# Optimization experiments

Hardware: AMD Instinct MI355X
Metric: run time of the kernel (lower is better)

## Reference

```python
import jax, jax.numpy as jnp
import numpy as np

F = 16        # num_frames
K = 8         # num_tokens (top-k)
SIZE = 64     # basis size
PD = 256      # prompt_dim
ED = 768      # embed_dim
EPS = 1e-12

def _l2norm(v, axis=-1):
    n = jnp.sqrt(jnp.sum(v * v, axis=axis, keepdims=True))
    return v / jnp.maximum(n, EPS)

def setup_inputs() -> dict:
    key = jax.random.key(0)
    k1, k2, k3, k4 = jax.random.split(key, 4)
    B, N = 32, 197
    x = jax.random.normal(k1, (B, F * N, ED), dtype=jnp.float32)
    # prompt_values ~ U(-1, 1), shape [size, 1, prompt_dim]
    prompt_values = jax.random.uniform(k2, (SIZE, 1, PD), dtype=jnp.float32, minval=-1.0, maxval=1.0)
    # prompt_inproj: Linear(embed_dim, prompt_dim, bias=False)
    W_in = jax.random.normal(k3, (PD, ED), dtype=jnp.float32) * (1.0 / np.sqrt(ED))
    # prompt_outproj: Linear(prompt_dim, embed_dim, bias=False), kaiming fan_out
    W_out = jax.random.normal(k4, (ED, PD), dtype=jnp.float32) * np.sqrt(2.0 / ED)
    return {"x": x, "W_in": W_in, "W_out": W_out, "prompt_values": prompt_values}

def reference(x, W_in, W_out, prompt_values):
    B = x.shape[0]
    x = jax.lax.stop_gradient(x)                       # x.detach()
    xf = x.reshape(B, F, -1, ED).mean(axis=2)          # [B, F, ED]
    query = jnp.einsum('bfe,pe->bfp', xf, W_in)        # prompt_inproj
    BZ = B * F
    q = _l2norm(query.reshape(BZ, PD), axis=1)         # [BZ, PD]
    keys = _l2norm(prompt_values.mean(axis=1), axis=1) # [SIZE, PD]
    sim = q @ keys.T                                   # [BZ, SIZE]
    # eval routing: top-k by similarity (argsort descending [:, :k])
    _, idx = jax.lax.top_k(sim, K)                     # [BZ, K] int32
    prompts = prompt_values[idx.reshape(-1)].reshape(BZ, K, PD)
    prompts = _l2norm(prompts, axis=-1)
    sel_sim = jnp.take_along_axis(sim, idx, axis=1)    # [BZ, K]
    sel_key = keys[idx]                                # [BZ, K, PD]
    recon = jnp.einsum('bk,bkd->bd', sel_sim, sel_key) # [BZ, PD]
    diff = jnp.sum((recon - jax.lax.stop_gradient(q)) ** 2) / BZ
    ksim = jnp.sum(jnp.abs(keys @ keys.T - jnp.eye(SIZE, dtype=keys.dtype))) / BZ
    ps = diff + ksim
    # rearrange '(b f) p d -> b (f p) d' then outproj
    out_prompts = prompts.reshape(B, F * K, PD)
    out_prompts = jnp.einsum('bnd,ed->bne', out_prompts, W_out)  # [B, F*K, ED]
    ps_loss = jnp.zeros((1,), dtype=x.dtype) + ps * F
    return out_prompts, ps_loss
```

## Files before the change

### kernel.cpp

```cpp
#include <hip/hip_runtime.h>

#define Ff 16
#define Kk 8
#define SIZEk 64
#define PDd 256
#define EDd 768
#define Nn 197
#define BZz 512
#define NPROD 64
#define RB  256
#define ED4 192
#define PD4 64
#define OUT_LOSS ((size_t)32 * 128 * EDd)
#define LOSS_SCALE (1.0f / 32.0f)
#define MAGIC 0x5A17EC0Du

__device__ __forceinline__ void acc4(float4& s, float4 a) {
    s.x += a.x; s.y += a.y; s.z += a.z; s.w += a.w;
}

__global__ __launch_bounds__(256, 2) void k_all(const float4* __restrict__ x,
                                                const float* __restrict__ Win,
                                                const float* __restrict__ Wout,
                                                const float* __restrict__ pv,
                                                float* __restrict__ keys,
                                                float* __restrict__ KW,
                                                unsigned* __restrict__ slots,
                                                float* __restrict__ out) {
    int blk = blockIdx.x, t = threadIdx.x;

    if (blk < NPROD) {
        __shared__ float ks[PDd];
        __shared__ float redp[4];
        __shared__ float s_norm;
        int s = blk;
        float v  = pv[(size_t)s * PDd + t];
        float sq = v * v;
        for (int o = 32; o > 0; o >>= 1) sq += __shfl_down(sq, o);
        if ((t & 63) == 0) redp[t >> 6] = sq;
        __syncthreads();
        if (t == 0) s_norm = fmaxf(sqrtf(redp[0] + redp[1] + redp[2] + redp[3]), 1e-12f);
        __syncthreads();
        float kv = v / s_norm;
        ks[t] = kv;
        keys[(size_t)s * PDd + t] = kv;
        __syncthreads();

        for (int r = 0; r < 3; r++) {
            int e = t + 256 * r;
            const float4* w  = (const float4*)(Wout + (size_t)e * PDd);
            const float4* k4 = (const float4*)ks;
            float d = 0.f;
            for (int i = 0; i < PD4; i++) {
                float4 wv = w[i]; float4 kvv = k4[i];
                d += wv.x * kvv.x + wv.y * kvv.y + wv.z * kvv.z + wv.w * kvv.w;
            }
            KW[(size_t)s * EDd + e] = d;
        }
        if (s == 0 && t == 0) out[OUT_LOSS] = 0.0f;
        __syncthreads();
        if (t == 0)
            __hip_atomic_store(&slots[s], MAGIC, __ATOMIC_RELEASE, __HIP_MEMORY_SCOPE_AGENT);

        if (t < SIZEk) {
            while (__hip_atomic_load(&slots[t], __ATOMIC_ACQUIRE, __HIP_MEMORY_SCOPE_AGENT)
                   != MAGIC)
                __builtin_amdgcn_s_sleep(8);
        }
        __syncthreads();
        if (t < SIZEk) {
            const float4* a = (const float4*)(keys + (size_t)s * PDd);
            const float4* b = (const float4*)(keys + (size_t)t * PDd);
            float d = 0.f;
            for (int c = 0; c < PD4; c++) {
                float4 av = a[c], bv = b[c];
                d += av.x * bv.x + av.y * bv.y + av.z * bv.z + av.w * bv.w;
            }
            float vv = fabsf(d - (s == t ? 1.0f : 0.0f));
            for (int o = 32; o > 0; o >>= 1) vv += __shfl_down(vv, o);
            if (t == 0) atomicAdd(out + OUT_LOSS, vv * LOSS_SCALE);
        }
        return;
    }

    __shared__ float xs[2][EDd];
    __shared__ float qs[2][PDd];
    __shared__ int   s_idx[2][Kk];
    __shared__ float s_sim[2][Kk];
    __shared__ float red[2][4];
    int bz0 = (blk - NPROD) * 2;

    {
        const float4* b0 = x + (size_t)bz0 * Nn * ED4;
        const float4* b1 = b0 + (size_t)Nn * ED4;
        const int  rA = (t < ED4) ? 0 : 1;
        const int  cA = (t < ED4) ? t : (t - ED4);
        const float4* pA = (rA ? b1 : b0) + cA;
        const bool hasB = (t < 128);
        const int  cB   = 64 + (t & 127);
        const float4* pB = b1 + cB;
        float4 sA = make_float4(0.f, 0.f, 0.f, 0.f);
        float4 sB = make_float4(0.f, 0.f, 0.f, 0.f);
        int n = 0;
        if (hasB) {
            for (; n + 8 <= Nn; n += 8) {
                float4 a0 = pA[(n + 0) * ED4], a1 = pA[(n + 1) * ED4];
                float4 a2 = pA[(n + 2) * ED4], a3 = pA[(n + 3) * ED4];
                float4 a4 = pA[(n + 4) * ED4], a5 = pA[(n + 5) * ED4];
                float4 a6 = pA[(n + 6) * ED4], a7 = pA[(n + 7) * ED4];
                float4 q0 = pB[(n + 0) * ED4], q1 = pB[(n + 1) * ED4];
                float4 q2 = pB[(n + 2) * ED4], q3 = pB[(n + 3) * ED4];
                float4 q4 = pB[(n + 4) * ED4], q5 = pB[(n + 5) * ED4];
                float4 q6 = pB[(n + 6) * ED4], q7 = pB[(n + 7) * ED4];
                acc4(sA, a0); acc4(sA, a1); acc4(sA, a2); acc4(sA, a3);
                acc4(sA, a4); acc4(sA, a5); acc4(sA, a6); acc4(sA, a7);
                acc4(sB, q0); acc4(sB, q1); acc4(sB, q2); acc4(sB, q3);
                acc4(sB, q4); acc4(sB, q5); acc4(sB, q6); acc4(sB, q7);
            }
            for (; n < Nn; n++) { acc4(sA, pA[n * ED4]); acc4(sB, pB[n * ED4]); }
        } else {
            for (; n + 8 <= Nn; n += 8) {
                float4 a0 = pA[(n + 0) * ED4], a1 = pA[(n + 1) * ED4];
                float4 a2 = pA[(n + 2) * ED4], a3 = pA[(n + 3) * ED4];
                float4 a4 = pA[(n + 4) * ED4], a5 = pA[(n + 5) * ED4];
                float4 a6 = pA[(n + 6) * ED4], a7 = pA[(n + 7) * ED4];
                acc4(sA, a0); acc4(sA, a1); acc4(sA, a2); acc4(sA, a3);
                acc4(sA, a4); acc4(sA, a5); acc4(sA, a6); acc4(sA, a7);
            }
            for (; n < Nn; n++) acc4(sA, pA[n * ED4]);
        }
        const float inv = 1.0f / (float)Nn;
        ((float4*)xs[rA])[cA] = make_float4(sA.x * inv, sA.y * inv, sA.z * inv, sA.w * inv);
        if (hasB)
            ((float4*)xs[1])[cB] = make_float4(sB.x * inv, sB.y * inv, sB.z * inv, sB.w * inv);
    }
    __syncthreads();

    {
        const float4* w  = (const float4*)Win + (size_t)t * ED4;
        const float4* x0 = (const float4*)xs[0];
        const float4* x1 = (const float4*)xs[1];
        float d0a = 0.f, d0b = 0.f, d1a = 0.f, d1b = 0.f;
        for (int i = 0; i < ED4; i += 2) {
            float4 w0 = w[i],     w1 = w[i + 1];
            float4 u0 = x0[i],    u1 = x1[i];
            float4 u2 = x0[i + 1], u3 = x1[i + 1];
            d0a += w0.x * u0.x + w0.y * u0.y + w0.z * u0.z + w0.w * u0.w;
            d1a += w0.x * u1.x + w0.y * u1.y + w0.z * u1.z + w0.w * u1.w;
            d0b += w1.x * u2.x + w1.y * u2.y + w1.z * u2.z + w1.w * u2.w;
            d1b += w1.x * u3.x + w1.y * u3.y + w1.z * u3.z + w1.w * u3.w;
        }
        float d0 = d0a + d0b, d1 = d1a + d1b;
        float sq0 = d0 * d0, sq1 = d1 * d1;
        for (int o = 32; o > 0; o >>= 1) {
            sq0 += __shfl_down(sq0, o);
            sq1 += __shfl_down(sq1, o);
        }
        if ((t & 63) == 0) { red[0][t >> 6] = sq0; red[1][t >> 6] = sq1; }
        __syncthreads();
        float n0 = fmaxf(sqrtf(red[0][0] + red[0][1] + red[0][2] + red[0][3]), 1e-12f);
        float n1 = fmaxf(sqrtf(red[1][0] + red[1][1] + red[1][2] + red[1][3]), 1e-12f);
        qs[0][t] = d0 / n0;
        qs[1][t] = d1 / n1;
    }

    if (t < SIZEk) {
        while (__hip_atomic_load(&slots[t], __ATOMIC_ACQUIRE, __HIP_MEMORY_SCOPE_AGENT)
               != MAGIC)
            __builtin_amdgcn_s_sleep(8);
    }
    __syncthreads();

    if (t < 2 * SIZEk) {
        int row  = t >> 6;
        int lane = t & 63;
        const float4* kr = (const float4*)(keys + (size_t)lane * PDd);
        const float4* qr = (const float4*)qs[row];
        float d = 0.f;
        for (int c = 0; c < PD4; c++) {
            float4 a = kr[c], b = qr[c];
            d += a.x * b.x + a.y * b.y + a.z * b.z + a.w * b.w;
        }
        float v = d;
        for (int k = 0; k < Kk; k++) {
            float mv = v; int mi = lane;
            for (int o = 32; o > 0; o >>= 1) {
                float ov = __shfl_xor(mv, o);
                int   oi = __shfl_xor(mi, o);
                if (ov > mv || (ov == mv && oi < mi)) { mv = ov; mi = oi; }
            }
            if (lane == 0) { s_idx[row][k] = mi; s_sim[row][k] = mv; }
            if (lane == mi) v = -3e38f;
        }
    }
    __syncthreads();

    {
        float r0 = 0.f, r1 = 0.f;
        for (int k = 0; k < Kk; k++) {
            r0 += s_sim[0][k] * keys[(size_t)s_idx[0][k] * PDd + t];
            r1 += s_sim[1][k] * keys[(size_t)s_idx[1][k] * PDd + t];
        }
        float e0 = r0 - qs[0][t];
        float e1 = r1 - qs[1][t];
        float sq = e0 * e0 + e1 * e1;
        for (int o = 32; o > 0; o >>= 1) sq += __shfl_down(sq, o);
        if ((t & 63) == 0) red[0][t >> 6] = sq;
        __syncthreads();
        if (t == 0) atomicAdd(out + OUT_LOSS,
                              (red[0][0] + red[0][1] + red[0][2] + red[0][3]) * LOSS_SCALE);
    }

    float4* orow = (float4*)out + (size_t)bz0 * Kk * ED4;
    for (int i = t; i < 2 * Kk * ED4; i += 256) {
        int which = i / ED4;
        int e4    = i - which * ED4;
        int idx   = s_idx[which >> 3][which & 7];
        orow[i] = ((const float4*)(KW + (size_t)idx * EDd))[e4];
    }
}

extern "C" void kernel_launch(void* const* d_in, const int* in_sizes, int n_in,
                              void* d_out, int out_size, void* d_ws, size_t ws_size,
                              hipStream_t stream) {
    const float* x    = (const float*)d_in[0];
    const float* Win  = (const float*)d_in[1];
    const float* Wout = (const float*)d_in[2];
    const float* pv   = (const float*)d_in[3];
    float* out = (float*)d_out;
    float* ws  = (float*)d_ws;

    float*    keys  = ws;
    float*    KW    = ws + 16384;
    unsigned* slots = (unsigned*)(ws + 65536);

    k_all<<<NPROD + RB, 256, 0, stream>>>((const float4*)x, Win, Wout, pv,
                                          keys, KW, slots, out);
}
```

Measured before the change: 502.9 us.

## Split frame-mean into a separate high-parallelism kernel before routing kernel

The single fused kernel is split into two launches. The first computes key normalisation plus the per-frame token mean, using 1536 blocks (three column chunks per frame, four row-groups per block). The second does the projection, top-k routing and output gather from the stored means. This spreads the ~194MB streaming read of x across many more blocks than the previous 256 to raise memory-level parallelism. It also removes the in-kernel spin-wait on key slots, at the cost of an extra launch and a small workspace round trip.

```diff
diff --git a/kernel.cpp b/kernel.cpp
--- a/kernel.cpp
+++ b/kernel.cpp
@@ -8,6 +8,7 @@
 #define Nn 197
 #define BZz 512
 #define NPROD 64
+#define NMEAN 1536
 #define RB  256
 #define ED4 192
 #define PD4 64
@@ -19,14 +20,14 @@
     s.x += a.x; s.y += a.y; s.z += a.z; s.w += a.w;
 }
 
-__global__ __launch_bounds__(256, 2) void k_all(const float4* __restrict__ x,
-                                                const float* __restrict__ Win,
-                                                const float* __restrict__ Wout,
-                                                const float* __restrict__ pv,
-                                                float* __restrict__ keys,
-                                                float* __restrict__ KW,
-                                                unsigned* __restrict__ slots,
-                                                float* __restrict__ out) {
+__global__ __launch_bounds__(256, 4) void k_mean(const float4* __restrict__ x,
+                                                 const float* __restrict__ Wout,
+                                                 const float* __restrict__ pv,
+                                                 float* __restrict__ keys,
+                                                 float* __restrict__ KW,
+                                                 unsigned* __restrict__ slots,
+                                                 float4* __restrict__ xf,
+                                                 float* __restrict__ out) {
     int blk = blockIdx.x, t = threadIdx.x;
 
     if (blk < NPROD) {
@@ -83,56 +84,57 @@
         return;
     }
 
+    int m  = blk - NPROD;
+    int bz = m / 3;
+    int c3 = m - bz * 3;
+    int c = t & 63, g = t >> 6;
+    const int STR = 4 * ED4;
+    const float4* p = x + ((size_t)bz * Nn + g) * ED4 + c3 * 64 + c;
+    float4 s = make_float4(0.f, 0.f, 0.f, 0.f);
+    int cnt = (Nn - g + 3) >> 2;
+    int j = 0;
+    for (; j + 8 <= cnt; j += 8) {
+        float4 a0 = p[(size_t)(j + 0) * STR], a1 = p[(size_t)(j + 1) * STR];
+        float4 a2 = p[(size_t)(j + 2) * STR], a3 = p[(size_t)(j + 3) * STR];
+        float4 a4 = p[(size_t)(j + 4) * STR], a5 = p[(size_t)(j + 5) * STR];
+        float4 a6 = p[(size_t)(j + 6) * STR], a7 = p[(size_t)(j + 7) * STR];
+        acc4(s, a0); acc4(s, a1); acc4(s, a2); acc4(s, a3);
+        acc4(s, a4); acc4(s, a5); acc4(s, a6); acc4(s, a7);
+    }
+    for (; j < cnt; j++) acc4(s, p[(size_t)j * STR]);
+
+    __shared__ float4 part[4][64];
+    part[g][c] = s;
+    __syncthreads();
+    if (t < 64) {
+        float4 a = part[0][t], b = part[1][t], d2 = part[2][t], e = part[3][t];
+        const float inv = 1.0f / (float)Nn;
+        float4 r;
+        r.x = (a.x + b.x + d2.x + e.x) * inv;
+        r.y = (a.y + b.y + d2.y + e.y) * inv;
+        r.z = (a.z + b.z + d2.z + e.z) * inv;
+        r.w = (a.w + b.w + d2.w + e.w) * inv;
+        xf[(size_t)bz * ED4 + c3 * 64 + t] = r;
+    }
+}
+
+__global__ __launch_bounds__(256, 2) void k_route(const float* __restrict__ Win,
+                                                  const float* __restrict__ keys,
+                                                  const float* __restrict__ KW,
+                                                  const float4* __restrict__ xf,
+                                                  float* __restrict__ out) {
+    int blk = blockIdx.x, t = threadIdx.x;
     __shared__ float xs[2][EDd];
     __shared__ float qs[2][PDd];
     __shared__ int   s_idx[2][Kk];
     __shared__ float s_sim[2][Kk];
     __shared__ float red[2][4];
-    int bz0 = (blk - NPROD) * 2;
+    int bz0 = blk * 2;
 
     {
-        const float4* b0 = x + (size_t)bz0 * Nn * ED4;
-        const float4* b1 = b0 + (size_t)Nn * ED4;
-        const int  rA = (t < ED4) ? 0 : 1;
-        const int  cA = (t < ED4) ? t : (t - ED4);
-        const float4* pA = (rA ? b1 : b0) + cA;
-        const bool hasB = (t < 128);
-        const int  cB   = 64 + (t & 127);
-        const float4* pB = b1 + cB;
-        float4 sA = make_float4(0.f, 0.f, 0.f, 0.f);
-        float4 sB = make_float4(0.f, 0.f, 0.f, 0.f);
-        int n = 0;
-        if (hasB) {
-            for (; n + 8 <= Nn; n += 8) {
-                float4 a0 = pA[(n + 0) * ED4], a1 = pA[(n + 1) * ED4];
-                float4 a2 = pA[(n + 2) * ED4], a3 = pA[(n + 3) * ED4];
-                float4 a4 = pA[(n + 4) * ED4], a5 = pA[(n + 5) * ED4];
-                float4 a6 = pA[(n + 6) * ED4], a7 = pA[(n + 7) * ED4];
-                float4 q0 = pB[(n + 0) * ED4], q1 = pB[(n + 1) * ED4];
-                float4 q2 = pB[(n + 2) * ED4], q3 = pB[(n + 3) * ED4];
-                float4 q4 = pB[(n + 4) * ED4], q5 = pB[(n + 5) * ED4];
-                float4 q6 = pB[(n + 6) * ED4], q7 = pB[(n + 7) * ED4];
-                acc4(sA, a0); acc4(sA, a1); acc4(sA, a2); acc4(sA, a3);
-                acc4(sA, a4); acc4(sA, a5); acc4(sA, a6); acc4(sA, a7);
-                acc4(sB, q0); acc4(sB, q1); acc4(sB, q2); acc4(sB, q3);
-                acc4(sB, q4); acc4(sB, q5); acc4(sB, q6); acc4(sB, q7);
-            }
-            for (; n < Nn; n++) { acc4(sA, pA[n * ED4]); acc4(sB, pB[n * ED4]); }
-        } else {
-            for (; n + 8 <= Nn; n += 8) {
-                float4 a0 = pA[(n + 0) * ED4], a1 = pA[(n + 1) * ED4];
-                float4 a2 = pA[(n + 2) * ED4], a3 = pA[(n + 3) * ED4];
-                float4 a4 = pA[(n + 4) * ED4], a5 = pA[(n + 5) * ED4];
-                float4 a6 = pA[(n + 6) * ED4], a7 = pA[(n + 7) * ED4];
-                acc4(sA, a0); acc4(sA, a1); acc4(sA, a2); acc4(sA, a3);
-                acc4(sA, a4); acc4(sA, a5); acc4(sA, a6); acc4(sA, a7);
-            }
-            for (; n < Nn; n++) acc4(sA, pA[n * ED4]);
-        }
-        const float inv = 1.0f / (float)Nn;
-        ((float4*)xs[rA])[cA] = make_float4(sA.x * inv, sA.y * inv, sA.z * inv, sA.w * inv);
-        if (hasB)
-            ((float4*)xs[1])[cB] = make_float4(sB.x * inv, sB.y * inv, sB.z * inv, sB.w * inv);
+        const float4* src = xf + (size_t)bz0 * ED4;
+        for (int i = t; i < 2 * ED4; i += 256)
+            ((float4*)xs)[i] = src[i];
     }
     __syncthreads();
 
@@ -142,8 +144,8 @@
         const float4* x1 = (const float4*)xs[1];
         float d0a = 0.f, d0b = 0.f, d1a = 0.f, d1b = 0.f;
         for (int i = 0; i < ED4; i += 2) {
-            float4 w0 = w[i],     w1 = w[i + 1];
-            float4 u0 = x0[i],    u1 = x1[i];
+            float4 w0 = w[i],      w1 = w[i + 1];
+            float4 u0 = x0[i],     u1 = x1[i];
             float4 u2 = x0[i + 1], u3 = x1[i + 1];
             d0a += w0.x * u0.x + w0.y * u0.y + w0.z * u0.z + w0.w * u0.w;
             d1a += w0.x * u1.x + w0.y * u1.y + w0.z * u1.z + w0.w * u1.w;
@@ -162,12 +164,6 @@
         float n1 = fmaxf(sqrtf(red[1][0] + red[1][1] + red[1][2] + red[1][3]), 1e-12f);
         qs[0][t] = d0 / n0;
         qs[1][t] = d1 / n1;
-    }
-
-    if (t < SIZEk) {
-        while (__hip_atomic_load(&slots[t], __ATOMIC_ACQUIRE, __HIP_MEMORY_SCOPE_AGENT)
-               != MAGIC)
-            __builtin_amdgcn_s_sleep(8);
     }
     __syncthreads();
 
@@ -233,7 +229,9 @@
     float*    keys  = ws;
     float*    KW    = ws + 16384;
     unsigned* slots = (unsigned*)(ws + 65536);
-
-    k_all<<<NPROD + RB, 256, 0, stream>>>((const float4*)x, Win, Wout, pv,
-                                          keys, KW, slots, out);
-}
+    float*    xf    = ws + 65600;
+
+    k_mean<<<NPROD + NMEAN, 256, 0, stream>>>((const float4*)x, Wout, pv,
+                                              keys, KW, slots, (float4*)xf, out);
+    k_route<<<RB, 256, 0, stream>>>(Win, keys, KW, (const float4*)xf, out);
+}
```

New measurement: 510.5 us. About the same (+1.5%).
